# Performance work log

Hardware: AMD Instinct MI355X
Metric: run time of the kernel (lower is better)

The kernel has to match this reference:

```python
import jax, jax.numpy as jnp
from jax import lax
import numpy as np

IOU_THRESHOLD = 0.35
SCORE_THRESHOLD = 0.5


def _pairwise_iou(b):
    # b: [N,4] boxes in (ymin, xmin, ymax, xmax) convention (tf boxes)
    y1, x1, y2, x2 = b[:, 0], b[:, 1], b[:, 2], b[:, 3]
    area = (y2 - y1) * (x2 - x1)
    iy1 = jnp.maximum(y1[:, None], y1[None, :])
    ix1 = jnp.maximum(x1[:, None], x1[None, :])
    iy2 = jnp.minimum(y2[:, None], y2[None, :])
    ix2 = jnp.minimum(x2[:, None], x2[None, :])
    inter = jnp.maximum(iy2 - iy1, 0.0) * jnp.maximum(ix2 - ix1, 0.0)
    union = area[:, None] + area[None, :] - inter
    return jnp.where(union > 0, inter / union, 0.0)  # [N,N]


def _nms_sample_image(scores, boxes, anchors_wh, num_samples):
    # scores [N], boxes [N,4], anchors_wh [N,2]
    N = scores.shape[0]
    order = jnp.argsort(-scores)  # descending by score, like tf NMS
    s = scores[order]
    b = boxes[order]
    a = anchors_wh[order]
    valid = s > SCORE_THRESHOLD
    iou = _pairwise_iou(b)  # [N,N] on score-sorted boxes
    idx = jnp.arange(N)

    # greedy suppression: box i kept iff valid and no earlier kept box overlaps > thr
    def step(keep, i):
        suppressed = jnp.any(keep & (idx < i) & (iou[i] > IOU_THRESHOLD))
        return keep.at[i].set(valid[i] & ~suppressed), None

    keep, _ = lax.scan(step, jnp.zeros(N, dtype=bool), idx)

    # gather kept entries in (descending-score) order, then pad/slice to num_samples
    rank = jnp.cumsum(keep) - 1  # output slot for each kept entry
    slot = jnp.where(keep, jnp.minimum(rank, num_samples), num_samples)
    vals = jnp.concatenate([s[:, None], b, a], axis=1)  # [N,7]
    out = jnp.zeros((num_samples + 1, 7), vals.dtype).at[slot].set(vals)
    return out[:num_samples]  # [num_samples, 7] = (score | box(4) | anchor_wh(2))


def reference(scores, boxes, anchors, num_samples):
    # scores [B,H,W,1], boxes [B,H,W,4], anchors [B,H,W,4] (last 2 chans = w,h)
    B = scores.shape[0]
    sc = scores.reshape(B, -1)
    bx = boxes.reshape(B, -1, 4)
    an = anchors[..., 2:].reshape(B, -1, 2)
    out = jax.vmap(lambda s, b, a: _nms_sample_image(s, b, a, num_samples))(sc, bx, an)
    return out  # [B, num_samples, 7]


def setup_inputs() -> dict:
    key = jax.random.key(0)
    k1, k2, k3, k4, k5 = jax.random.split(key, 5)
    B, H, W = 8, 64, 64
    scores = jax.random.uniform(k1, (B, H, W, 1), dtype=jnp.float32)
    # well-formed tf boxes: ymin<ymax, xmin<xmax in [0,1]
    ymin = jax.random.uniform(k2, (B, H, W, 1), dtype=jnp.float32) * 0.8
    xmin = jax.random.uniform(k3, (B, H, W, 1), dtype=jnp.float32) * 0.8
    hh = jax.random.uniform(k4, (B, H, W, 1), dtype=jnp.float32) * 0.18 + 0.02
    ww = jax.random.uniform(k5, (B, H, W, 1), dtype=jnp.float32) * 0.18 + 0.02
    boxes = jnp.concatenate([ymin, xmin, ymin + hh, xmin + ww], axis=-1)
    # anchors: [cy, cx, w, h]-style; only last two channels are used
    k6 = jax.random.fold_in(key, 6)
    anchors = jax.random.uniform(k6, (B, H, W, 4), dtype=jnp.float32) * 0.25 + 0.05
    return {"scores": scores, "boxes": boxes, "anchors": anchors, "num_samples": 300}
```

## Files before the change

### kernel.cpp

```cpp
#include <hip/hip_runtime.h>

static constexpr float kIouT = 0.35f;
static constexpr float kScoreT = 0.5f;
static constexpr int kMaxKeep = 512;

__device__ __forceinline__ float iou_f(const float4 a, const float4 b) {
  float areaA = __fmul_rn(a.z - a.x, a.w - a.y);
  float areaB = __fmul_rn(b.z - b.x, b.w - b.y);
  float iy1 = fmaxf(a.x, b.x);
  float ix1 = fmaxf(a.y, b.y);
  float iy2 = fminf(a.z, b.z);
  float ix2 = fminf(a.w, b.w);
  float dy = fmaxf(iy2 - iy1, 0.0f);
  float dx = fmaxf(ix2 - ix1, 0.0f);
  float inter = __fmul_rn(dy, dx);
  float uni = (areaA + areaB) - inter;
  return (uni > 0.0f) ? __fdiv_rn(inter, uni) : 0.0f;
}

__device__ __forceinline__ unsigned long long rdlane64(unsigned long long v,
                                                       int l) {
  unsigned lo = (unsigned)__builtin_amdgcn_readlane((int)(unsigned)v, l);
  unsigned hi = (unsigned)__builtin_amdgcn_readlane((int)(unsigned)(v >> 32), l);
  return ((unsigned long long)hi << 32) | lo;
}

__global__ __launch_bounds__(256)
void nms_rank_kernel(const float* __restrict__ scores,
                     const float4* __restrict__ boxes,
                     unsigned long long* __restrict__ skeys,
                     float4* __restrict__ sboxes,
                     int* __restrict__ Mcnt, int N, int rankBlocks) {
  const int tid = threadIdx.x;
  const int lane = tid & 63;
  if ((int)blockIdx.x >= rankBlocks) {
    __shared__ int part[4];
    const int img = blockIdx.x - rankBlocks;
    const int wv = tid >> 6;
    const float4* sc4 = (const float4*)(scores + (size_t)img * N);
    int c = 0;
    for (int q = tid; q < (N >> 2); q += 256) {
      float4 v = sc4[q];
      c += (v.x > kScoreT) + (v.y > kScoreT) + (v.z > kScoreT) + (v.w > kScoreT);
    }
#pragma unroll
    for (int off = 1; off < 64; off <<= 1) c += __shfl_xor(c, off, 64);
    if (lane == 0) part[wv] = c;
    __syncthreads();
    if (tid == 0) Mcnt[img] = part[0] + part[1] + part[2] + part[3];
    return;
  }
  const int wid = (int)(((unsigned)blockIdx.x * blockDim.x + tid) >> 6);
  const int img = wid / N;
  const int row = wid - img * N;
  const float* sc = scores + (size_t)img * N;
  const float si = sc[row];
  if (!(si > kScoreT)) return;
  const float4* sc4 = (const float4*)sc;
  int cnt = 0;
  for (int q = lane; q < (N >> 2); q += 64) {
    const float4 v = sc4[q];
    const int j = q << 2;
    cnt += (v.x > si) + (v.y > si) + (v.z > si) + (v.w > si);
    if (v.x == si && j < row) cnt++;
    if (v.y == si && j + 1 < row) cnt++;
    if (v.z == si && j + 2 < row) cnt++;
    if (v.w == si && j + 3 < row) cnt++;
  }
#pragma unroll
  for (int off = 1; off < 64; off <<= 1) cnt += __shfl_xor(cnt, off, 64);
  if (lane == 0) {
    skeys[(size_t)img * N + cnt] =
        ((unsigned long long)(~__float_as_uint(si)) << 32) | (unsigned)row;
    sboxes[(size_t)img * N + cnt] = boxes[(size_t)img * N + row];
  }
}

__global__ __launch_bounds__(256)
void nms_mask_kernel(const float4* __restrict__ sboxes,
                     const int* __restrict__ Mcnt,
                     unsigned long long* __restrict__ mask,
                     int N, int totalRows) {
  const int wid = (int)(((unsigned)blockIdx.x * blockDim.x + threadIdx.x) >> 6);
  const int lane = threadIdx.x & 63;
  if (wid >= totalRows) return;
  const int img = wid / N;
  const int row = wid - img * N;
  const int m = Mcnt[img];
  if (row >= m) return;
  const float4* sb = sboxes + (size_t)img * N;
  const float4 bi = sb[row];
  const int nw = (m + 63) >> 6;
  unsigned long long* mrow = mask + (size_t)wid * (size_t)(N >> 6);
  for (int w = row >> 6; w < nw; ++w) {
    int j = (w << 6) | lane;
    bool sup = false;
    if (j > row && j < m) sup = iou_f(bi, sb[j]) > kIouT;
    unsigned long long bm = __ballot(sup);
    if (lane == 0) mrow[w] = bm;
  }
}

__global__ __launch_bounds__(64, 1)
void nms_scan_kernel(const unsigned long long* __restrict__ skeys,
                     const float4* __restrict__ sboxes,
                     const int* __restrict__ Mcnt,
                     const unsigned long long* __restrict__ mask,
                     const float* __restrict__ anchors,
                     float* __restrict__ out, int N, int NS) {
  __shared__ int keptlist[kMaxKeep];
  const int img = blockIdx.x;
  const int lane = threadIdx.x;
  int m = Mcnt[img];
  if (m > N) m = N;
  const int nw = (m + 63) >> 6;
  const int stride = N >> 6;
  const unsigned long long* mbase = mask + (size_t)img * (size_t)N * stride;
  const unsigned long long* kg = skeys + (size_t)img * N;
  const float4* sb = sboxes + (size_t)img * N;
  const float* an = anchors + (size_t)img * (size_t)N * 4;
  float* o = out + (size_t)img * NS * 7;

  int kept = 0;
  unsigned long long remv = 0ull;

  if (m > 0) {
    auto dgload = [&](int cc) -> unsigned long long {
      const int cl = cc < (nw - 1) ? cc : (nw - 1);
      return mbase[(size_t)((cl << 6) + lane) * stride + cl];
    };
    unsigned long long dg0 = dgload(0);
    unsigned long long dg1 = dgload(1);
    unsigned long long dg2 = dgload(2);

    for (int c = 0; c < nw && kept < NS; ++c) {
      const int cb = c << 6;
      unsigned long long local = rdlane64(remv, c);
      const int rem = m - cb;
      unsigned long long avail = ~local;
      if (rem < 64) avail &= (1ull << rem) - 1ull;
      unsigned long long keptbits = 0ull;
      const int keptbase = kept;
      while (avail != 0ull && kept < NS) {
        const int b = (int)__builtin_ctzll(avail);
        keptbits |= 1ull << b;
        kept++;
        const unsigned long long rc = rdlane64(dg0, b);
        local |= rc;
        avail &= ~local;
        avail &= ~(1ull << b);
      }
      dg0 = dg1; dg1 = dg2; dg2 = dgload(c + 3);
      if (keptbits != 0ull) {
        if (lane == 0) {
          unsigned long long kl = keptbits;
          int kc = keptbase;
          while (kl != 0ull) {
            const int b = (int)__builtin_ctzll(kl);
            kl &= kl - 1ull;
            keptlist[kc++] = cb + b;
          }
        }
        if (kept < NS || c + 1 < nw) {
          const bool lok = (lane > c) && (lane < nw);
          unsigned long long kb = keptbits;
          while (kb != 0ull) {
            int bs[16];
            int bcur = (int)__builtin_ctzll(kb);
#pragma unroll
            for (int k = 0; k < 16; ++k) {
              if (kb != 0ull) {
                bcur = (int)__builtin_ctzll(kb);
                kb &= kb - 1ull;
              }
              bs[k] = bcur;
            }
            unsigned long long t[16];
#pragma unroll
            for (int k = 0; k < 16; ++k)
              t[k] = mbase[(size_t)(cb + bs[k]) * stride + lane];
            unsigned long long acc = 0ull;
#pragma unroll
            for (int k = 0; k < 16; ++k) acc |= t[k];
            if (lok) remv |= acc;
          }
        }
      }
    }
  }

  __syncthreads();
  for (int t = lane; t < kept; t += 64) {
    const int i = keptlist[t];
    const unsigned long long ki = kg[i];
    const float4 bi = sb[i];
    const unsigned idx = (unsigned)ki;
    float* row = o + t * 7;
    row[0] = __uint_as_float(~(unsigned)(ki >> 32));
    row[1] = bi.x; row[2] = bi.y; row[3] = bi.z; row[4] = bi.w;
    row[5] = an[idx * 4 + 2];
    row[6] = an[idx * 4 + 3];
  }
  for (int t = kept * 7 + lane; t < NS * 7; t += 64) o[t] = 0.0f;
}

__global__ __launch_bounds__(1024)
void nms_fused_kernel(const float* __restrict__ scores,
                      const float4* __restrict__ boxes,
                      const float* __restrict__ anchors,
                      float* __restrict__ out, int N, int NS) {
  __shared__ unsigned long long keys[4096];
  __shared__ int s_m;
  if (N > 4096) return;
  const int img = blockIdx.x;
  const int tid = threadIdx.x;
  const float* sc = scores + (size_t)img * N;
  const float4* bx = boxes + (size_t)img * N;
  if (tid == 0) s_m = 0;
  __syncthreads();
  int cnt = 0;
  for (int i = tid; i < N; i += blockDim.x) {
    float s = sc[i];
    keys[i] = ((unsigned long long)(~__float_as_uint(s)) << 32) | (unsigned)i;
    if (s > kScoreT) cnt++;
  }
  if (cnt) atomicAdd(&s_m, cnt);
  __syncthreads();
  for (int k = 2; k <= N; k <<= 1) {
    for (int j = k >> 1; j > 0; j >>= 1) {
      for (int i = tid; i < N; i += blockDim.x) {
        int ixj = i ^ j;
        if (ixj > i) {
          unsigned long long a = keys[i];
          unsigned long long b = keys[ixj];
          bool up = ((i & k) == 0);
          if (up ? (a > b) : (a < b)) { keys[i] = b; keys[ixj] = a; }
        }
      }
      __syncthreads();
    }
  }
  if (tid >= 64) return;
  const int lane = tid;
  const int m = s_m;
  const int nw = (m + 63) >> 6;
  const float* an = anchors + (size_t)img * N * 4;
  float* o = out + (size_t)img * NS * 7;
  unsigned long long remv = 0ull;
  int kept = 0;
  for (int i = 0; i < m && kept < NS; ++i) {
    unsigned long long rw = __shfl(remv, i >> 6, 64);
    if ((rw >> (i & 63)) & 1ull) continue;
    unsigned long long ki = keys[i];
    float4 bi = bx[(unsigned)ki];
    if (lane == 0) {
      unsigned idx = (unsigned)ki;
      float* row = o + kept * 7;
      row[0] = __uint_as_float(~(unsigned)(ki >> 32));
      row[1] = bi.x; row[2] = bi.y; row[3] = bi.z; row[4] = bi.w;
      row[5] = an[idx * 4 + 2];
      row[6] = an[idx * 4 + 3];
    }
    kept++;
    for (int w2 = i >> 6; w2 < nw; ++w2) {
      int j = (w2 << 6) | lane;
      bool sup = false;
      if (j > i && j < m) sup = iou_f(bi, bx[(unsigned)keys[j]]) > kIouT;
      unsigned long long bm = __ballot(sup);
      if (lane == w2) remv |= bm;
    }
  }
  for (int t = kept * 7 + lane; t < NS * 7; t += 64) o[t] = 0.0f;
}

extern "C" void kernel_launch(void* const* d_in, const int* in_sizes, int n_in,
                              void* d_out, int out_size, void* d_ws, size_t ws_size,
                              hipStream_t stream) {
  const float* scores = (const float*)d_in[0];
  const float4* boxes = (const float4*)d_in[1];
  const float* anchors = (const float*)d_in[2];
  float* out = (float*)d_out;
  const int B = 8;
  const int N = in_sizes[0] / B;
  const int NS = out_size / (B * 7);

  const size_t nTot = (size_t)B * (size_t)N;
  const size_t keysB = nTot * 8;
  const size_t sboxB = nTot * 16;
  const size_t mcntB = 256;
  const size_t maskB = nTot * (size_t)(N >> 6) * 8;
  const size_t need = keysB + sboxB + mcntB + maskB;

  if (ws_size >= need && (N % 256) == 0 && N >= 256 && N <= 4096 &&
      NS <= kMaxKeep) {
    char* p = (char*)d_ws;
    unsigned long long* skeys = (unsigned long long*)p; p += keysB;
    float4* sboxes = (float4*)p;                         p += sboxB;
    int* Mcnt = (int*)p;                                 p += mcntB;
    unsigned long long* mask = (unsigned long long*)p;

    const int totalRows = B * N;
    const int rankBlocks = totalRows / 4;
    nms_rank_kernel<<<rankBlocks + B, 256, 0, stream>>>(scores, boxes, skeys,
                                                        sboxes, Mcnt, N,
                                                        rankBlocks);
    nms_mask_kernel<<<rankBlocks, 256, 0, stream>>>(sboxes, Mcnt, mask, N,
                                                    totalRows);
    nms_scan_kernel<<<B, 64, 0, stream>>>(skeys, sboxes, Mcnt, mask, anchors,
                                          out, N, NS);
  } else {
    nms_fused_kernel<<<B, 1024, 0, stream>>>(scores, boxes, anchors, out, N, NS);
  }
}
```

Before: 95.30 us.

## Recompute diagonal and next-chunk IoU in scan, defer mask-row loads

The serial scan kernel no longer loads the diagonal mask block from global memory. It recomputes intra-chunk suppression with readlane-broadcast boxes and a ballot, and it computes suppression of the next chunk directly from boxes. Mask-row loads for the kept boxes are deferred by one chunk through a pending register array, so their latency overlaps the next chunk's work. An early-exit IoU predicate also skips the division when boxes do not overlap. This trades global-load latency on the serial critical path for extra ALU work and more register pressure.

```diff
diff --git a/kernel.cpp b/kernel.cpp
--- a/kernel.cpp
+++ b/kernel.cpp
@@ -18,11 +18,26 @@
   return (uni > 0.0f) ? __fdiv_rn(inter, uni) : 0.0f;
 }
 
+__device__ __forceinline__ bool iou_gt(const float4 a, const float4 b) {
+  const float iy1 = fmaxf(a.x, b.x), ix1 = fmaxf(a.y, b.y);
+  const float iy2 = fminf(a.z, b.z), ix2 = fminf(a.w, b.w);
+  const float dy = iy2 - iy1, dx = ix2 - ix1;
+  if (!(dy > 0.0f && dx > 0.0f)) return false;
+  const float inter = __fmul_rn(dy, dx);
+  const float aA = __fmul_rn(a.z - a.x, a.w - a.y);
+  const float aB = __fmul_rn(b.z - b.x, b.w - b.y);
+  const float uni = (aA + aB) - inter;
+  return (uni > 0.0f) && (__fdiv_rn(inter, uni) > kIouT);
+}
+
 __device__ __forceinline__ unsigned long long rdlane64(unsigned long long v,
                                                        int l) {
   unsigned lo = (unsigned)__builtin_amdgcn_readlane((int)(unsigned)v, l);
   unsigned hi = (unsigned)__builtin_amdgcn_readlane((int)(unsigned)(v >> 32), l);
   return ((unsigned long long)hi << 32) | lo;
+}
+__device__ __forceinline__ float rdlane_f(float v, int l) {
+  return __int_as_float(__builtin_amdgcn_readlane(__float_as_int(v), l));
 }
 
 __global__ __launch_bounds__(256)
@@ -113,6 +128,7 @@
   const int lane = threadIdx.x;
   int m = Mcnt[img];
   if (m > N) m = N;
+  if (m < 0) m = 0;
   const int nw = (m + 63) >> 6;
   const int stride = N >> 6;
   const unsigned long long* mbase = mask + (size_t)img * (size_t)N * stride;
@@ -122,70 +138,93 @@
   float* o = out + (size_t)img * NS * 7;
 
   int kept = 0;
-  unsigned long long remv = 0ull;
-
   if (m > 0) {
-    auto dgload = [&](int cc) -> unsigned long long {
-      const int cl = cc < (nw - 1) ? cc : (nw - 1);
-      return mbase[(size_t)((cl << 6) + lane) * stride + cl];
+    auto bxload = [&](int cc) -> float4 {
+      int idx = (cc << 6) + lane;
+      if (idx >= m) idx = m - 1;
+      return sb[idx];
     };
-    unsigned long long dg0 = dgload(0);
-    unsigned long long dg1 = dgload(1);
-    unsigned long long dg2 = dgload(2);
+    float4 bx0 = bxload(0);
+    float4 bx1 = bxload(1);
+    float4 bx2 = bxload(2);
+    unsigned long long pend[16];
+    int pendn = 0, pendc = 0;
+    unsigned long long remv = 0ull, nextw = 0ull;
 
     for (int c = 0; c < nw && kept < NS; ++c) {
       const int cb = c << 6;
-      unsigned long long local = rdlane64(remv, c);
+      unsigned long long local = rdlane64(remv, c) | nextw;
       const int rem = m - cb;
       unsigned long long avail = ~local;
       if (rem < 64) avail &= (1ull << rem) - 1ull;
       unsigned long long keptbits = 0ull;
-      const int keptbase = kept;
       while (avail != 0ull && kept < NS) {
         const int b = (int)__builtin_ctzll(avail);
+        keptlist[kept] = cb + b;
+        kept++;
         keptbits |= 1ull << b;
-        kept++;
-        const unsigned long long rc = rdlane64(dg0, b);
+        const float4 bb = {rdlane_f(bx0.x, b), rdlane_f(bx0.y, b),
+                           rdlane_f(bx0.z, b), rdlane_f(bx0.w, b)};
+        const bool sup = (lane > b) && iou_gt(bb, bx0);
+        const unsigned long long rc = __ballot(sup);
         local |= rc;
         avail &= ~local;
         avail &= ~(1ull << b);
       }
-      dg0 = dg1; dg1 = dg2; dg2 = dgload(c + 3);
-      if (keptbits != 0ull) {
-        if (lane == 0) {
-          unsigned long long kl = keptbits;
-          int kc = keptbase;
-          while (kl != 0ull) {
-            const int b = (int)__builtin_ctzll(kl);
-            kl &= kl - 1ull;
-            keptlist[kc++] = cb + b;
+      {
+        const bool lok = (lane >= pendc) && (lane < nw);
+#pragma unroll
+        for (int k = 0; k < 16; ++k)
+          if (k < pendn && lok) remv |= pend[k];
+      }
+      unsigned long long kb = keptbits;
+      int nk = (int)__popcll(keptbits);
+      while (nk > 16) {
+        int bs[16];
+#pragma unroll
+        for (int k = 0; k < 16; ++k) {
+          bs[k] = (int)__builtin_ctzll(kb);
+          kb &= kb - 1ull;
+        }
+        unsigned long long tt[16];
+#pragma unroll
+        for (int k = 0; k < 16; ++k)
+          tt[k] = mbase[(size_t)(cb + bs[k]) * stride + lane];
+        unsigned long long acc = 0ull;
+#pragma unroll
+        for (int k = 0; k < 16; ++k) acc |= tt[k];
+        if (lane >= c && lane < nw) remv |= acc;
+        nk -= 16;
+      }
+      pendn = nk;
+      pendc = c;
+      if (nk > 0) {
+        int bs[16];
+        int bcur = (int)__builtin_ctzll(kb);
+#pragma unroll
+        for (int k = 0; k < 16; ++k) {
+          if (kb != 0ull) {
+            bcur = (int)__builtin_ctzll(kb);
+            kb &= kb - 1ull;
           }
+          bs[k] = bcur;
         }
-        if (kept < NS || c + 1 < nw) {
-          const bool lok = (lane > c) && (lane < nw);
-          unsigned long long kb = keptbits;
-          while (kb != 0ull) {
-            int bs[16];
-            int bcur = (int)__builtin_ctzll(kb);
-#pragma unroll
-            for (int k = 0; k < 16; ++k) {
-              if (kb != 0ull) {
-                bcur = (int)__builtin_ctzll(kb);
-                kb &= kb - 1ull;
-              }
-              bs[k] = bcur;
-            }
-            unsigned long long t[16];
-#pragma unroll
-            for (int k = 0; k < 16; ++k)
-              t[k] = mbase[(size_t)(cb + bs[k]) * stride + lane];
-            unsigned long long acc = 0ull;
-#pragma unroll
-            for (int k = 0; k < 16; ++k) acc |= t[k];
-            if (lok) remv |= acc;
-          }
-        }
-      }
+#pragma unroll
+        for (int k = 0; k < 16; ++k)
+          pend[k] = mbase[(size_t)(cb + bs[k]) * stride + lane];
+      }
+      nextw = 0ull;
+      kb = keptbits;
+      while (kb != 0ull) {
+        const int b = (int)__builtin_ctzll(kb);
+        kb &= kb - 1ull;
+        const float4 bb = {rdlane_f(bx0.x, b), rdlane_f(bx0.y, b),
+                           rdlane_f(bx0.z, b), rdlane_f(bx0.w, b)};
+        nextw |= __ballot(iou_gt(bb, bx1));
+      }
+      bx0 = bx1;
+      bx1 = bx2;
+      bx2 = bxload(c + 3);
     }
   }
 
@@ -265,7 +304,7 @@
     for (int w2 = i >> 6; w2 < nw; ++w2) {
       int j = (w2 << 6) | lane;
       bool sup = false;
-      if (j > i && j < m) sup = iou_f(bi, bx[(unsigned)keys[j]]) > kIouT;
+      if (j > i && j < m) sup = iou_gt(bi, bx[(unsigned)keys[j]]);
       unsigned long long bm = __ballot(sup);
       if (lane == w2) remv |= bm;
     }
```

Measured after the change: 176.7 us. 85.4% more time.

## Add helper waves to prefetch mask rows into cache during serial NMS scan

Applied to the files above, without the earlier changes.

The scan kernel now launches 512 threads. Wave 0 runs the serial greedy scan at raised priority. The other seven waves stream every mask row the scan may later read, so those rows are warm in L2 when wave 0 gathers them. This targets the latency of the dependent global loads in the serial scan, at the cost of extra memory traffic and possible contention with the critical wave. The fallback fused kernel also gains an early-out IoU test, but that path does not run for this input shape.

```diff
diff --git a/kernel.cpp b/kernel.cpp
--- a/kernel.cpp
+++ b/kernel.cpp
@@ -16,6 +16,18 @@
   float inter = __fmul_rn(dy, dx);
   float uni = (areaA + areaB) - inter;
   return (uni > 0.0f) ? __fdiv_rn(inter, uni) : 0.0f;
+}
+
+__device__ __forceinline__ bool iou_gt(const float4 a, const float4 b) {
+  const float iy1 = fmaxf(a.x, b.x), ix1 = fmaxf(a.y, b.y);
+  const float iy2 = fminf(a.z, b.z), ix2 = fminf(a.w, b.w);
+  const float dy = iy2 - iy1, dx = ix2 - ix1;
+  if (!(dy > 0.0f && dx > 0.0f)) return false;
+  const float inter = __fmul_rn(dy, dx);
+  const float aA = __fmul_rn(a.z - a.x, a.w - a.y);
+  const float aB = __fmul_rn(b.z - b.x, b.w - b.y);
+  const float uni = (aA + aB) - inter;
+  return (uni > 0.0f) && (__fdiv_rn(inter, uni) > kIouT);
 }
 
 __device__ __forceinline__ unsigned long long rdlane64(unsigned long long v,
@@ -101,7 +113,7 @@
   }
 }
 
-__global__ __launch_bounds__(64, 1)
+__global__ __launch_bounds__(512, 1)
 void nms_scan_kernel(const unsigned long long* __restrict__ skeys,
                      const float4* __restrict__ sboxes,
                      const int* __restrict__ Mcnt,
@@ -109,10 +121,14 @@
                      const float* __restrict__ anchors,
                      float* __restrict__ out, int N, int NS) {
   __shared__ int keptlist[kMaxKeep];
+  __shared__ int s_kept;
   const int img = blockIdx.x;
-  const int lane = threadIdx.x;
+  const int tid = threadIdx.x;
+  const int lane = tid & 63;
+  const int wv = tid >> 6;
   int m = Mcnt[img];
   if (m > N) m = N;
+  if (m < 0) m = 0;
   const int nw = (m + 63) >> 6;
   const int stride = N >> 6;
   const unsigned long long* mbase = mask + (size_t)img * (size_t)N * stride;
@@ -121,76 +137,99 @@
   const float* an = anchors + (size_t)img * (size_t)N * 4;
   float* o = out + (size_t)img * NS * 7;
 
-  int kept = 0;
-  unsigned long long remv = 0ull;
-
-  if (m > 0) {
-    auto dgload = [&](int cc) -> unsigned long long {
-      const int cl = cc < (nw - 1) ? cc : (nw - 1);
-      return mbase[(size_t)((cl << 6) + lane) * stride + cl];
-    };
-    unsigned long long dg0 = dgload(0);
-    unsigned long long dg1 = dgload(1);
-    unsigned long long dg2 = dgload(2);
-
-    for (int c = 0; c < nw && kept < NS; ++c) {
-      const int cb = c << 6;
-      unsigned long long local = rdlane64(remv, c);
-      const int rem = m - cb;
-      unsigned long long avail = ~local;
-      if (rem < 64) avail &= (1ull << rem) - 1ull;
-      unsigned long long keptbits = 0ull;
-      const int keptbase = kept;
-      while (avail != 0ull && kept < NS) {
-        const int b = (int)__builtin_ctzll(avail);
-        keptbits |= 1ull << b;
-        kept++;
-        const unsigned long long rc = rdlane64(dg0, b);
-        local |= rc;
-        avail &= ~local;
-        avail &= ~(1ull << b);
-      }
-      dg0 = dg1; dg1 = dg2; dg2 = dgload(c + 3);
-      if (keptbits != 0ull) {
-        if (lane == 0) {
-          unsigned long long kl = keptbits;
-          int kc = keptbase;
-          while (kl != 0ull) {
-            const int b = (int)__builtin_ctzll(kl);
-            kl &= kl - 1ull;
-            keptlist[kc++] = cb + b;
+  if (wv == 0) {
+    __builtin_amdgcn_s_setprio(1);
+    int kept = 0;
+    unsigned long long remv = 0ull;
+    if (m > 0) {
+      auto dgload = [&](int cc) -> unsigned long long {
+        const int cl = cc < (nw - 1) ? cc : (nw - 1);
+        return mbase[(size_t)((cl << 6) + lane) * stride + cl];
+      };
+      unsigned long long dg0 = dgload(0);
+      unsigned long long dg1 = dgload(1);
+      unsigned long long dg2 = dgload(2);
+
+      for (int c = 0; c < nw && kept < NS; ++c) {
+        const int cb = c << 6;
+        unsigned long long local = rdlane64(remv, c);
+        const int rem = m - cb;
+        unsigned long long avail = ~local;
+        if (rem < 64) avail &= (1ull << rem) - 1ull;
+        unsigned long long keptbits = 0ull;
+        const int keptbase = kept;
+        while (avail != 0ull && kept < NS) {
+          const int b = (int)__builtin_ctzll(avail);
+          keptbits |= 1ull << b;
+          kept++;
+          const unsigned long long rc = rdlane64(dg0, b);
+          local |= rc;
+          avail &= ~local;
+          avail &= ~(1ull << b);
+        }
+        dg0 = dg1; dg1 = dg2; dg2 = dgload(c + 3);
+        if (keptbits != 0ull) {
+          if (lane == 0) {
+            unsigned long long kl = keptbits;
+            int kc = keptbase;
+            while (kl != 0ull) {
+              const int b = (int)__builtin_ctzll(kl);
+              kl &= kl - 1ull;
+              keptlist[kc++] = cb + b;
+            }
           }
-        }
-        if (kept < NS || c + 1 < nw) {
-          const bool lok = (lane > c) && (lane < nw);
-          unsigned long long kb = keptbits;
-          while (kb != 0ull) {
-            int bs[16];
-            int bcur = (int)__builtin_ctzll(kb);
-#pragma unroll
-            for (int k = 0; k < 16; ++k) {
-              if (kb != 0ull) {
-                bcur = (int)__builtin_ctzll(kb);
-                kb &= kb - 1ull;
+          if (kept < NS || c + 1 < nw) {
+            const bool lok = (lane > c) && (lane < nw);
+            unsigned long long kb = keptbits;
+            while (kb != 0ull) {
+              int bs[16];
+              int bcur = (int)__builtin_ctzll(kb);
+#pragma unroll
+              for (int k = 0; k < 16; ++k) {
+                if (kb != 0ull) {
+                  bcur = (int)__builtin_ctzll(kb);
+                  kb &= kb - 1ull;
+                }
+                bs[k] = bcur;
               }
-              bs[k] = bcur;
+              unsigned long long t[16];
+#pragma unroll
+              for (int k = 0; k < 16; ++k)
+                t[k] = mbase[(size_t)(cb + bs[k]) * stride + lane];
+              unsigned long long acc = 0ull;
+#pragma unroll
+              for (int k = 0; k < 16; ++k) acc |= t[k];
+              if (lok) remv |= acc;
             }
-            unsigned long long t[16];
-#pragma unroll
-            for (int k = 0; k < 16; ++k)
-              t[k] = mbase[(size_t)(cb + bs[k]) * stride + lane];
-            unsigned long long acc = 0ull;
-#pragma unroll
-            for (int k = 0; k < 16; ++k) acc |= t[k];
-            if (lok) remv |= acc;
           }
         }
       }
     }
+    if (lane == 0) s_kept = kept;
+    __builtin_amdgcn_s_setprio(0);
+  } else {
+    unsigned long long a0 = 0ull, a1 = 0ull, a2 = 0ull, a3 = 0ull;
+    const int r0 = wv - 1;
+    for (int r = r0; r < m; r += 28) {
+      const int ra = r, rb = r + 7, rc2 = r + 14, rd = r + 21;
+      if (lane < nw) {
+        if (ra < m && lane >= (ra >> 6))
+          a0 |= mbase[(size_t)ra * stride + lane];
+        if (rb < m && lane >= (rb >> 6))
+          a1 |= mbase[(size_t)rb * stride + lane];
+        if (rc2 < m && lane >= (rc2 >> 6))
+          a2 |= mbase[(size_t)rc2 * stride + lane];
+        if (rd < m && lane >= (rd >> 6))
+          a3 |= mbase[(size_t)rd * stride + lane];
+      }
+    }
+    a0 |= a1 | a2 | a3;
+    asm volatile("" ::"v"(a0));
   }
 
   __syncthreads();
-  for (int t = lane; t < kept; t += 64) {
+  const int K = s_kept;
+  for (int t = tid; t < K; t += 512) {
     const int i = keptlist[t];
     const unsigned long long ki = kg[i];
     const float4 bi = sb[i];
@@ -201,7 +240,7 @@
     row[5] = an[idx * 4 + 2];
     row[6] = an[idx * 4 + 3];
   }
-  for (int t = kept * 7 + lane; t < NS * 7; t += 64) o[t] = 0.0f;
+  for (int t = K * 7 + tid; t < NS * 7; t += 512) o[t] = 0.0f;
 }
 
 __global__ __launch_bounds__(1024)
@@ -265,7 +304,7 @@
     for (int w2 = i >> 6; w2 < nw; ++w2) {
       int j = (w2 << 6) | lane;
       bool sup = false;
-      if (j > i && j < m) sup = iou_f(bi, bx[(unsigned)keys[j]]) > kIouT;
+      if (j > i && j < m) sup = iou_gt(bi, bx[(unsigned)keys[j]]);
       unsigned long long bm = __ballot(sup);
       if (lane == w2) remv |= bm;
     }
@@ -306,8 +345,8 @@
                                                         rankBlocks);
     nms_mask_kernel<<<rankBlocks, 256, 0, stream>>>(sboxes, Mcnt, mask, N,
                                                     totalRows);
-    nms_scan_kernel<<<B, 64, 0, stream>>>(skeys, sboxes, Mcnt, mask, anchors,
-                                          out, N, NS);
+    nms_scan_kernel<<<B, 512, 0, stream>>>(skeys, sboxes, Mcnt, mask, anchors,
+                                           out, N, NS);
   } else {
     nms_fused_kernel<<<B, 1024, 0, stream>>>(scores, boxes, anchors, out, N, NS);
   }
```

Measured after the change: 145.2 us. +52.4%, slower.
